# Optimization experiments

Hardware: AMD Instinct MI355X
Metric: run time of the kernel (lower is better)

The kernel has to match this reference:

```python
import jax, jax.numpy as jnp
import numpy as np

EPS = 1e-8

def setup_inputs() -> dict:
    key = jax.random.key(0)
    k1, k2 = jax.random.split(key)
    B, N, D, K = 8, 8192, 768, 256
    x = jax.random.normal(k1, (B, N, D), dtype=jnp.float32)
    centers = jax.random.normal(k2, (B, K, D), dtype=jnp.float32)
    return {"x": x, "centers": centers}

def reference(x, centers):
    # tokens_norm / centers_norm as in the torch module (add-eps normalization)
    tn = x / (jnp.linalg.norm(x, axis=-1, keepdims=True) + EPS)
    cn = centers / (jnp.linalg.norm(centers, axis=-1, keepdims=True) + EPS)
    # F.cosine_similarity re-normalizes with clamp(norm, min=eps)
    tn2 = tn / jnp.maximum(jnp.linalg.norm(tn, axis=-1, keepdims=True), EPS)
    cn2 = cn / jnp.maximum(jnp.linalg.norm(cn, axis=-1, keepdims=True), EPS)
    # fused: cosine similarity via plain matmul instead of (B,N,K,D) broadcast
    cos_sim = jnp.einsum('bnd,bkd->bnk', tn2, cn2)  # (B,N,K)
    dist = 1.0 - cos_sim
    prob = jax.nn.softmax(-dist, axis=-1)  # softmax over K
    # weighted aggregation over N: (B,K,D)
    num = jnp.einsum('bnk,bnd->bkd', prob, x)
    den = jnp.sum(prob, axis=1)[..., None] + EPS  # (B,K,1)
    return num / den
```

## Files before the change

### kernel.cpp

```cpp
#include <hip/hip_runtime.h>
#include <hip/hip_bf16.h>

typedef __attribute__((ext_vector_type(8))) short bf16x8;
typedef __attribute__((ext_vector_type(4))) float f32x4;
typedef unsigned short u16;
typedef unsigned int u32;

__device__ __forceinline__ u16 f2bf(float f) {
    u32 u = __float_as_uint(f);
    u = (u + 0x7FFFu + ((u >> 16) & 1u)) >> 16;
    return (u16)u;
}
__device__ __forceinline__ u32 pk2(float a, float b) {
    return (u32)f2bf(a) | ((u32)f2bf(b) << 16);
}

#define GLDS16(g, l) __builtin_amdgcn_global_load_lds( \
    (const __attribute__((address_space(1))) u32*)(g), \
    (__attribute__((address_space(3))) u32*)(l), 16, 0, 0)

__global__ __launch_bounds__(256) void k_centers(const float* __restrict__ c, u16* __restrict__ cn) {
    int bid = blockIdx.x;
    int w = threadIdx.x >> 6, lane = threadIdx.x & 63;
    int row = (bid << 2) + w;
    int b = row >> 8;
    __shared__ u16 rb[4][800];
    const float* src = c + (size_t)row * 768;
    float v[12]; float ss = 0.f;
#pragma unroll
    for (int j = 0; j < 12; ++j) { v[j] = src[lane + (j << 6)]; ss += v[j] * v[j]; }
#pragma unroll
    for (int m = 1; m < 64; m <<= 1) ss += __shfl_xor(ss, m, 64);
    float inv = 1.0f / sqrtf(ss);
#pragma unroll
    for (int j = 0; j < 12; ++j) rb[w][lane + (j << 6)] = f2bf(v[j] * inv);
    __syncthreads();
    int t = threadIdx.x;
    int k0 = (bid << 2) & 255;
#pragma unroll
    for (int p = 0; p < 2; ++p) {
        int idx = (p << 8) + t;
        if (idx < 384) {
            int g = idx >> 2, kr = idx & 3;
            uint4 val = *reinterpret_cast<const uint4*>(&rb[kr][g << 3]);
            int kb = g >> 2, dc = g & 3;
            size_t o = ((((size_t)(b * 24 + kb) << 2) + dc) << 8) + k0 + kr;
            *reinterpret_cast<uint4*>(cn + (o << 3)) = val;
        }
    }
}

__global__ __launch_bounds__(256, 2) void k_gemm1(const float* __restrict__ x, const u16* __restrict__ cn,
                                                  u16* __restrict__ probT, float* __restrict__ den) {
    const int b = blockIdx.y;
    const int n0 = blockIdx.x << 7;
    const int t = threadIdx.x;
    const int wave = t >> 6, lane = t & 63;
    const int lg = lane >> 4, lr = lane & 15;
    const int wm = wave >> 1, wk = wave & 1;
    const int tok0 = wm << 6;
    const int kb0 = wk << 7;

    __shared__ union {
        struct {
            u16 A[2][4][130][8];
            u16 B[2][4][256][8];
        } s;
        u16 T[256][136];
    } u;
    __shared__ float inv_s[128];
    __shared__ float ksum[2][128];
    __shared__ float denp[256];

    denp[t] = 0.f;

    f32x4 acc[8][4];
#pragma unroll
    for (int kf = 0; kf < 8; ++kf)
#pragma unroll
        for (int tf = 0; tf < 4; ++tf) acc[kf][tf] = (f32x4){0.f, 0.f, 0.f, 0.f};

    const char* cnb = (const char*)(cn + (size_t)b * 24 * 4 * 256 * 8);
    const int tokS = ((t >> 1) & 63) + ((t >> 7) << 6);
    const int dcS = t & 1;
    const float* ap = x + ((size_t)b * 8192 + n0 + tokS) * 768 + (dcS << 3);

    float sq = 0.f;
    float4 f0, f1, f2, f3;

    auto issueA = [&](int kb) {
        const float* p = ap + (kb << 5);
        f0 = *reinterpret_cast<const float4*>(p);
        f1 = *reinterpret_cast<const float4*>(p + 4);
        f2 = *reinterpret_cast<const float4*>(p + 16);
        f3 = *reinterpret_cast<const float4*>(p + 20);
    };
    auto writeA = [&](int buf) {
        sq += f0.x*f0.x + f0.y*f0.y + f0.z*f0.z + f0.w*f0.w
            + f1.x*f1.x + f1.y*f1.y + f1.z*f1.z + f1.w*f1.w
            + f2.x*f2.x + f2.y*f2.y + f2.z*f2.z + f2.w*f2.w
            + f3.x*f3.x + f3.y*f3.y + f3.z*f3.z + f3.w*f3.w;
        *reinterpret_cast<uint4*>(&u.s.A[buf][dcS][tokS][0]) =
            make_uint4(pk2(f0.x, f0.y), pk2(f0.z, f0.w), pk2(f1.x, f1.y), pk2(f1.z, f1.w));
        *reinterpret_cast<uint4*>(&u.s.A[buf][dcS + 2][tokS][0]) =
            make_uint4(pk2(f2.x, f2.y), pk2(f2.z, f2.w), pk2(f3.x, f3.y), pk2(f3.z, f3.w));
    };
    auto issueB = [&](int buf, int kb) {
        const char* src = cnb + (size_t)kb * 16384 + (wave << 12) + (lane << 4);
        char* dst = (char*)&u.s.B[buf][0][0][0] + (wave << 12);
        GLDS16(src, dst);
        GLDS16(src + 1024, dst + 1024);
        GLDS16(src + 2048, dst + 2048);
        GLDS16(src + 3072, dst + 3072);
    };

    issueA(0); issueB(0, 0);
    writeA(0);
    __syncthreads();

    for (int kb = 0; kb < 24; ++kb) {
        int cur = kb & 1, nxt = cur ^ 1;
        if (kb < 23) { issueA(kb + 1); issueB(nxt, kb + 1); }
        bf16x8 a[4];
#pragma unroll
        for (int tf = 0; tf < 4; ++tf)
            a[tf] = *reinterpret_cast<const bf16x8*>(&u.s.A[cur][lg][tok0 + (tf << 4) + lr][0]);
#pragma unroll
        for (int kf = 0; kf < 8; ++kf) {
            bf16x8 bb = *reinterpret_cast<const bf16x8*>(&u.s.B[cur][lg][kb0 + (kf << 4) + lr][0]);
#pragma unroll
            for (int tf = 0; tf < 4; ++tf)
                acc[kf][tf] = __builtin_amdgcn_mfma_f32_16x16x32_bf16(a[tf], bb, acc[kf][tf], 0, 0, 0);
        }
        if (kb < 23) writeA(nxt);
        __syncthreads();
    }

    sq += __shfl_xor(sq, 1, 64);
    if ((t & 1) == 0) inv_s[tokS] = 1.0f / sqrtf(sq);
    __syncthreads();

    float iv[4][4];
#pragma unroll
    for (int tf = 0; tf < 4; ++tf)
#pragma unroll
        for (int r = 0; r < 4; ++r)
            iv[tf][r] = inv_s[tok0 + (tf << 4) + (lg << 2) + r];

    float rowsum[4][4];
#pragma unroll
    for (int tf = 0; tf < 4; ++tf)
#pragma unroll
        for (int r = 0; r < 4; ++r) rowsum[tf][r] = 0.f;
#pragma unroll
    for (int kf = 0; kf < 8; ++kf)
#pragma unroll
        for (int tf = 0; tf < 4; ++tf)
#pragma unroll
            for (int r = 0; r < 4; ++r) {
                float e = __expf(acc[kf][tf][r] * iv[tf][r]);
                acc[kf][tf][r] = e; rowsum[tf][r] += e;
            }
#pragma unroll
    for (int tf = 0; tf < 4; ++tf)
#pragma unroll
        for (int r = 0; r < 4; ++r) {
#pragma unroll
            for (int m = 1; m < 16; m <<= 1) rowsum[tf][r] += __shfl_xor(rowsum[tf][r], m, 64);
        }
    if (lr == 0) {
#pragma unroll
        for (int tf = 0; tf < 4; ++tf)
#pragma unroll
            for (int r = 0; r < 4; ++r)
                ksum[wk][tok0 + (tf << 4) + (lg << 2) + r] = rowsum[tf][r];
    }
    __syncthreads();

    float rs[4][4];
#pragma unroll
    for (int tf = 0; tf < 4; ++tf)
#pragma unroll
        for (int r = 0; r < 4; ++r) {
            int idx = tok0 + (tf << 4) + (lg << 2) + r;
            rs[tf][r] = 1.0f / (ksum[0][idx] + ksum[1][idx]);
        }

    float dcol[8];
#pragma unroll
    for (int kf = 0; kf < 8; ++kf) dcol[kf] = 0.f;
#pragma unroll
    for (int kf = 0; kf < 8; ++kf)
#pragma unroll
        for (int tf = 0; tf < 4; ++tf)
#pragma unroll
            for (int r = 0; r < 4; ++r) {
                float p = acc[kf][tf][r] * rs[tf][r];
                acc[kf][tf][r] = p; dcol[kf] += p;
            }
#pragma unroll
    for (int kf = 0; kf < 8; ++kf) {
        dcol[kf] += __shfl_xor(dcol[kf], 16, 64);
        dcol[kf] += __shfl_xor(dcol[kf], 32, 64);
    }
    if (lg == 0) {
#pragma unroll
        for (int kf = 0; kf < 8; ++kf) atomicAdd(&denp[kb0 + (kf << 4) + lr], dcol[kf]);
    }
#pragma unroll
    for (int kf = 0; kf < 8; ++kf)
#pragma unroll
        for (int tf = 0; tf < 4; ++tf)
            *reinterpret_cast<ushort4*>(&u.T[kb0 + (kf << 4) + lr][tok0 + (tf << 4) + (lg << 2)]) =
                make_ushort4(f2bf(acc[kf][tf][0]), f2bf(acc[kf][tf][1]),
                             f2bf(acc[kf][tf][2]), f2bf(acc[kf][tf][3]));
    __syncthreads();

    u16* pTb = probT + (size_t)b * 256 * 8192 + n0;
#pragma unroll
    for (int i = 0; i < 16; ++i) {
        int idx = (i << 8) + t;
        int row = idx >> 4, ch = idx & 15;
        *reinterpret_cast<uint4*>(pTb + (size_t)row * 8192 + (ch << 3)) =
            *reinterpret_cast<const uint4*>(&u.T[row][ch << 3]);
    }
    atomicAdd(&den[(b << 8) + t], denp[t]);
}

__global__ __launch_bounds__(256) void k_gemm2(const float* __restrict__ x, const u16* __restrict__ probT,
                                               float* __restrict__ num_part) {
    const int bid = blockIdx.x;
    const int xcd = bid & 7, slot = bid >> 3;
    const int orig = xcd * 96 + slot;
    const int dt = orig % 12, sb = orig / 12;
    const int s = sb >> 3, b = sb & 7;
    const int d0 = dt << 6;
    const int t = threadIdx.x;
    const int wave = t >> 6, lane = t & 63;
    const int lg = lane >> 4, lr = lane & 15;

    f32x4 acc[4][4];
#pragma unroll
    for (int m = 0; m < 4; ++m)
#pragma unroll
        for (int tt = 0; tt < 4; ++tt) acc[m][tt] = (f32x4){0.f, 0.f, 0.f, 0.f};

    const int n0 = s << 10;
    const u16* pA = probT + (size_t)b * 256 * 8192;
    const float* xB = x + (size_t)b * 8192 * 768;

    for (int kb = 0; kb < 32; ++kb) {
        int nbase = n0 + (kb << 5);
        bf16x8 a[4];
#pragma unroll
        for (int m = 0; m < 4; ++m) {
            int k = (wave << 6) + (m << 4) + lr;
            a[m] = *reinterpret_cast<const bf16x8*>(pA + (size_t)k * 8192 + nbase + (lg << 3));
        }
        const float* xr = xB + (size_t)(nbase + (lg << 3)) * 768 + d0 + lr;
        bf16x8 bb[4];
#pragma unroll
        for (int tt = 0; tt < 4; ++tt)
#pragma unroll
            for (int j = 0; j < 8; ++j) {
                float f = xr[(size_t)j * 768 + (tt << 4)];
                bb[tt][j] = (short)f2bf(f);
            }
#pragma unroll
        for (int m = 0; m < 4; ++m)
#pragma unroll
            for (int tt = 0; tt < 4; ++tt)
                acc[m][tt] = __builtin_amdgcn_mfma_f32_16x16x32_bf16(a[m], bb[tt], acc[m][tt], 0, 0, 0);
    }

    float* np = num_part + ((size_t)s * 8 + b) * 256 * 768;
#pragma unroll
    for (int m = 0; m < 4; ++m) {
        int kb_ = (wave << 6) + (m << 4) + (lg << 2);
#pragma unroll
        for (int reg = 0; reg < 4; ++reg)
#pragma unroll
            for (int tt = 0; tt < 4; ++tt)
                np[(size_t)(kb_ + reg) * 768 + d0 + (tt << 4) + lr] = acc[m][tt][reg];
    }
}

__global__ __launch_bounds__(256) void k_final(const float* __restrict__ num_part, const float* __restrict__ den,
                                               float* __restrict__ out) {
    int i = blockIdx.x * 256 + threadIdx.x;
    float sum = 0.f;
#pragma unroll
    for (int ss = 0; ss < 8; ++ss) sum += num_part[(size_t)ss * 1572864 + i];
    out[i] = sum / (den[i / 768] + 1e-8f);
}

extern "C" void kernel_launch(void* const* d_in, const int* in_sizes, int n_in,
                              void* d_out, int out_size, void* d_ws, size_t ws_size,
                              hipStream_t stream) {
    const float* x = (const float*)d_in[0];
    const float* centers = (const float*)d_in[1];
    float* out = (float*)d_out;
    char* ws = (char*)d_ws;
    u16* cn       = (u16*)ws;
    u16* probT    = (u16*)(ws + 3145728);
    float* den    = (float*)(ws + 36700160);
    float* numpt  = (float*)(ws + 36708352);

    hipMemsetAsync(den, 0, 8192, stream);
    k_centers<<<512, 256, 0, stream>>>(centers, cn);
    k_gemm1<<<dim3(64, 8), 256, 0, stream>>>(x, cn, probT, den);
    k_gemm2<<<768, 256, 0, stream>>>(x, probT, numpt);
    k_final<<<6144, 256, 0, stream>>>(numpt, den, out);
}
```

Before: 177.8 us.

## Enlarge gemm1 token tile to 256 with triple-buffered pipeline and partial-waitcnt barriers

k_gemm1 now processes 256 tokens per block with 512 threads. Each centers tile is therefore reused across twice as many tokens, and the grid is halved. The K loop is unrolled by two over a three-slot LDS ring. Custom barriers wait only until the newest stage's global loads remain outstanding (vmcnt(6)), so loads for step k+2 overlap MFMA work on step k. The transposed output buffer grows to about 135KB of LDS, which limits occupancy to one block per CU and relies on the hand-counted vmcnt being correct.

Measured after the change: 180.7 us. Within noise of the previous version (+1.6%).

```diff
diff --git a/kernel.cpp b/kernel.cpp
--- a/kernel.cpp
+++ b/kernel.cpp
@@ -18,6 +18,11 @@
 #define GLDS16(g, l) __builtin_amdgcn_global_load_lds( \
     (const __attribute__((address_space(1))) u32*)(g), \
     (__attribute__((address_space(3))) u32*)(l), 16, 0, 0)
+
+#define BAR_CNT6() do { asm volatile("s_waitcnt vmcnt(6) lgkmcnt(0)" ::: "memory"); \
+    __builtin_amdgcn_sched_barrier(0); __builtin_amdgcn_s_barrier(); } while (0)
+#define BAR_CNT0() do { asm volatile("s_waitcnt vmcnt(0) lgkmcnt(0)" ::: "memory"); \
+    __builtin_amdgcn_sched_barrier(0); __builtin_amdgcn_s_barrier(); } while (0)
 
 __global__ __launch_bounds__(256) void k_centers(const float* __restrict__ c, u16* __restrict__ cn) {
     int bid = blockIdx.x;
@@ -50,10 +55,10 @@
     }
 }
 
-__global__ __launch_bounds__(256, 2) void k_gemm1(const float* __restrict__ x, const u16* __restrict__ cn,
+__global__ __launch_bounds__(512, 2) void k_gemm1(const float* __restrict__ x, const u16* __restrict__ cn,
                                                   u16* __restrict__ probT, float* __restrict__ den) {
     const int b = blockIdx.y;
-    const int n0 = blockIdx.x << 7;
+    const int n0 = blockIdx.x << 8;
     const int t = threadIdx.x;
     const int wave = t >> 6, lane = t & 63;
     const int lg = lane >> 4, lr = lane & 15;
@@ -63,16 +68,16 @@
 
     __shared__ union {
         struct {
-            u16 A[2][4][130][8];
-            u16 B[2][4][256][8];
+            u16 A[3][4][258][8];
+            u16 B[3][4][256][8];
         } s;
-        u16 T[256][136];
+        u16 T[256][264];
     } u;
-    __shared__ float inv_s[128];
-    __shared__ float ksum[2][128];
+    __shared__ float inv_s[256];
+    __shared__ float ksum[2][256];
     __shared__ float denp[256];
 
-    denp[t] = 0.f;
+    if (t < 256) denp[t] = 0.f;
 
     f32x4 acc[8][4];
 #pragma unroll
@@ -81,59 +86,66 @@
         for (int tf = 0; tf < 4; ++tf) acc[kf][tf] = (f32x4){0.f, 0.f, 0.f, 0.f};
 
     const char* cnb = (const char*)(cn + (size_t)b * 24 * 4 * 256 * 8);
-    const int tokS = ((t >> 1) & 63) + ((t >> 7) << 6);
+    const int tokS = t >> 1;
     const int dcS = t & 1;
-    const float* ap = x + ((size_t)b * 8192 + n0 + tokS) * 768 + (dcS << 3);
+    const float* ap = x + ((size_t)b * 8192 + n0 + tokS) * 768 + (dcS << 4);
 
     float sq = 0.f;
-    float4 f0, f1, f2, f3;
-
-    auto issueA = [&](int kb) {
+    float4 fE[4], fO[4];
+
+    auto issueA = [&](int kb, float4* f) {
         const float* p = ap + (kb << 5);
-        f0 = *reinterpret_cast<const float4*>(p);
-        f1 = *reinterpret_cast<const float4*>(p + 4);
-        f2 = *reinterpret_cast<const float4*>(p + 16);
-        f3 = *reinterpret_cast<const float4*>(p + 20);
+        f[0] = *reinterpret_cast<const float4*>(p);
+        f[1] = *reinterpret_cast<const float4*>(p + 4);
+        f[2] = *reinterpret_cast<const float4*>(p + 8);
+        f[3] = *reinterpret_cast<const float4*>(p + 12);
     };
-    auto writeA = [&](int buf) {
-        sq += f0.x*f0.x + f0.y*f0.y + f0.z*f0.z + f0.w*f0.w
-            + f1.x*f1.x + f1.y*f1.y + f1.z*f1.z + f1.w*f1.w
-            + f2.x*f2.x + f2.y*f2.y + f2.z*f2.z + f2.w*f2.w
-            + f3.x*f3.x + f3.y*f3.y + f3.z*f3.z + f3.w*f3.w;
-        *reinterpret_cast<uint4*>(&u.s.A[buf][dcS][tokS][0]) =
-            make_uint4(pk2(f0.x, f0.y), pk2(f0.z, f0.w), pk2(f1.x, f1.y), pk2(f1.z, f1.w));
-        *reinterpret_cast<uint4*>(&u.s.A[buf][dcS + 2][tokS][0]) =
-            make_uint4(pk2(f2.x, f2.y), pk2(f2.z, f2.w), pk2(f3.x, f3.y), pk2(f3.z, f3.w));
+    auto writeA = [&](int buf, float4* f) {
+#pragma unroll
+        for (int j = 0; j < 4; ++j)
+            sq += f[j].x * f[j].x + f[j].y * f[j].y + f[j].z * f[j].z + f[j].w * f[j].w;
+        *reinterpret_cast<uint4*>(&u.s.A[buf][(dcS << 1) + 0][tokS][0]) =
+            make_uint4(pk2(f[0].x, f[0].y), pk2(f[0].z, f[0].w), pk2(f[1].x, f[1].y), pk2(f[1].z, f[1].w));
+        *reinterpret_cast<uint4*>(&u.s.A[buf][(dcS << 1) + 1][tokS][0]) =
+            make_uint4(pk2(f[2].x, f[2].y), pk2(f[2].z, f[2].w), pk2(f[3].x, f[3].y), pk2(f[3].z, f[3].w));
     };
     auto issueB = [&](int buf, int kb) {
-        const char* src = cnb + (size_t)kb * 16384 + (wave << 12) + (lane << 4);
-        char* dst = (char*)&u.s.B[buf][0][0][0] + (wave << 12);
+        const char* src = cnb + (size_t)kb * 16384 + (wave << 11) + (lane << 4);
+        char* dst = (char*)&u.s.B[buf][0][0][0] + (wave << 11);
         GLDS16(src, dst);
         GLDS16(src + 1024, dst + 1024);
-        GLDS16(src + 2048, dst + 2048);
-        GLDS16(src + 3072, dst + 3072);
     };
-
-    issueA(0); issueB(0, 0);
-    writeA(0);
-    __syncthreads();
-
-    for (int kb = 0; kb < 24; ++kb) {
-        int cur = kb & 1, nxt = cur ^ 1;
-        if (kb < 23) { issueA(kb + 1); issueB(nxt, kb + 1); }
+    auto mfmaStep = [&](int buf) {
         bf16x8 a[4];
 #pragma unroll
         for (int tf = 0; tf < 4; ++tf)
-            a[tf] = *reinterpret_cast<const bf16x8*>(&u.s.A[cur][lg][tok0 + (tf << 4) + lr][0]);
+            a[tf] = *reinterpret_cast<const bf16x8*>(&u.s.A[buf][lg][tok0 + (tf << 4) + lr][0]);
 #pragma unroll
         for (int kf = 0; kf < 8; ++kf) {
-            bf16x8 bb = *reinterpret_cast<const bf16x8*>(&u.s.B[cur][lg][kb0 + (kf << 4) + lr][0]);
+            bf16x8 bb = *reinterpret_cast<const bf16x8*>(&u.s.B[buf][lg][kb0 + (kf << 4) + lr][0]);
 #pragma unroll
             for (int tf = 0; tf < 4; ++tf)
                 acc[kf][tf] = __builtin_amdgcn_mfma_f32_16x16x32_bf16(a[tf], bb, acc[kf][tf], 0, 0, 0);
         }
-        if (kb < 23) writeA(nxt);
-        __syncthreads();
+    };
+
+    issueA(0, fE); issueB(0, 0);
+    issueA(1, fO); issueB(1, 1);
+    writeA(0, fE);
+    BAR_CNT6();
+
+    for (int kb = 0; kb < 24; kb += 2) {
+        int bi0 = kb % 3, bi1 = (kb + 1) % 3, bi2 = (kb + 2) % 3;
+        if (kb < 22) { issueA(kb + 2, fE); issueB(bi2, kb + 2); }
+        mfmaStep(bi0);
+        writeA(bi1, fO);
+        BAR_CNT6();
+        if (kb < 21) { issueA(kb + 3, fO); issueB(bi0, kb + 3); }
+        mfmaStep(bi1);
+        if (kb < 22) {
+            writeA(bi2, fE);
+            if (kb == 20) { BAR_CNT0(); } else { BAR_CNT6(); }
+        }
     }
 
     sq += __shfl_xor(sq, 1, 64);
@@ -219,12 +231,12 @@
     u16* pTb = probT + (size_t)b * 256 * 8192 + n0;
 #pragma unroll
     for (int i = 0; i < 16; ++i) {
-        int idx = (i << 8) + t;
-        int row = idx >> 4, ch = idx & 15;
+        int idx = (i << 9) + t;
+        int row = idx >> 5, ch = idx & 31;
         *reinterpret_cast<uint4*>(pTb + (size_t)row * 8192 + (ch << 3)) =
             *reinterpret_cast<const uint4*>(&u.T[row][ch << 3]);
     }
-    atomicAdd(&den[(b << 8) + t], denp[t]);
+    if (t < 256) atomicAdd(&den[(b << 8) + t], denp[t]);
 }
 
 __global__ __launch_bounds__(256) void k_gemm2(const float* __restrict__ x, const u16* __restrict__ probT,
@@ -308,7 +320,7 @@
 
     hipMemsetAsync(den, 0, 8192, stream);
     k_centers<<<512, 256, 0, stream>>>(centers, cn);
-    k_gemm1<<<dim3(64, 8), 256, 0, stream>>>(x, cn, probT, den);
+    k_gemm1<<<dim3(32, 8), 512, 0, stream>>>(x, cn, probT, den);
     k_gemm2<<<768, 256, 0, stream>>>(x, probT, numpt);
     k_final<<<6144, 256, 0, stream>>>(numpt, den, out);
 }
```

## Restructure gemm1 to load operands directly into registers with smaller tiles

Applied to the files above, without the earlier changes.

Rewrites the first GEMM kernel so each block handles 64 tokens instead of 128, and each wave owns a 64-wide slice of the 256 centers. The shared-memory staging, double buffering and global_load_lds path are removed, and fragments are loaded straight from global memory into registers. The grid becomes 1024 blocks interleaved across batches, with a higher occupancy bound. This cuts LDS use and barriers to raise occupancy. In exchange, every wave re-reads the same x rows from global or cache, and loads are no longer software-pipelined.

Result: slower. 246.4 us (+38.6%).

```diff
diff --git a/kernel.cpp b/kernel.cpp
--- a/kernel.cpp
+++ b/kernel.cpp
@@ -14,10 +14,7 @@
 __device__ __forceinline__ u32 pk2(float a, float b) {
     return (u32)f2bf(a) | ((u32)f2bf(b) << 16);
 }
-
-#define GLDS16(g, l) __builtin_amdgcn_global_load_lds( \
-    (const __attribute__((address_space(1))) u32*)(g), \
-    (__attribute__((address_space(3))) u32*)(l), 16, 0, 0)
+union B8 { u32 u[4]; bf16x8 v; };
 
 __global__ __launch_bounds__(256) void k_centers(const float* __restrict__ c, u16* __restrict__ cn) {
     int bid = blockIdx.x;
@@ -50,179 +47,149 @@
     }
 }
 
-__global__ __launch_bounds__(256, 2) void k_gemm1(const float* __restrict__ x, const u16* __restrict__ cn,
+__global__ __launch_bounds__(256, 3) void k_gemm1(const float* __restrict__ x, const u16* __restrict__ cn,
                                                   u16* __restrict__ probT, float* __restrict__ den) {
-    const int b = blockIdx.y;
-    const int n0 = blockIdx.x << 7;
+    const int bid = blockIdx.x;
+    const int b = bid & 7;
+    const int n0 = (bid >> 3) << 6;
     const int t = threadIdx.x;
     const int wave = t >> 6, lane = t & 63;
     const int lg = lane >> 4, lr = lane & 15;
-    const int wm = wave >> 1, wk = wave & 1;
-    const int tok0 = wm << 6;
-    const int kb0 = wk << 7;
-
-    __shared__ union {
-        struct {
-            u16 A[2][4][130][8];
-            u16 B[2][4][256][8];
-        } s;
-        u16 T[256][136];
-    } u;
-    __shared__ float inv_s[128];
-    __shared__ float ksum[2][128];
+    const int kq = wave << 6;
+
+    __shared__ u16 T[256][72];
+    __shared__ float inv_s[64];
+    __shared__ float ksum[4][64];
     __shared__ float denp[256];
 
-    denp[t] = 0.f;
-
-    f32x4 acc[8][4];
-#pragma unroll
-    for (int kf = 0; kf < 8; ++kf)
-#pragma unroll
-        for (int tf = 0; tf < 4; ++tf) acc[kf][tf] = (f32x4){0.f, 0.f, 0.f, 0.f};
-
-    const char* cnb = (const char*)(cn + (size_t)b * 24 * 4 * 256 * 8);
-    const int tokS = ((t >> 1) & 63) + ((t >> 7) << 6);
-    const int dcS = t & 1;
-    const float* ap = x + ((size_t)b * 8192 + n0 + tokS) * 768 + (dcS << 3);
-
-    float sq = 0.f;
-    float4 f0, f1, f2, f3;
-
-    auto issueA = [&](int kb) {
-        const float* p = ap + (kb << 5);
-        f0 = *reinterpret_cast<const float4*>(p);
-        f1 = *reinterpret_cast<const float4*>(p + 4);
-        f2 = *reinterpret_cast<const float4*>(p + 16);
-        f3 = *reinterpret_cast<const float4*>(p + 20);
-    };
-    auto writeA = [&](int buf) {
-        sq += f0.x*f0.x + f0.y*f0.y + f0.z*f0.z + f0.w*f0.w
-            + f1.x*f1.x + f1.y*f1.y + f1.z*f1.z + f1.w*f1.w
-            + f2.x*f2.x + f2.y*f2.y + f2.z*f2.z + f2.w*f2.w
-            + f3.x*f3.x + f3.y*f3.y + f3.z*f3.z + f3.w*f3.w;
-        *reinterpret_cast<uint4*>(&u.s.A[buf][dcS][tokS][0]) =
-            make_uint4(pk2(f0.x, f0.y), pk2(f0.z, f0.w), pk2(f1.x, f1.y), pk2(f1.z, f1.w));
-        *reinterpret_cast<uint4*>(&u.s.A[buf][dcS + 2][tokS][0]) =
-            make_uint4(pk2(f2.x, f2.y), pk2(f2.z, f2.w), pk2(f3.x, f3.y), pk2(f3.z, f3.w));
-    };
-    auto issueB = [&](int buf, int kb) {
-        const char* src = cnb + (size_t)kb * 16384 + (wave << 12) + (lane << 4);
-        char* dst = (char*)&u.s.B[buf][0][0][0] + (wave << 12);
-        GLDS16(src, dst);
-        GLDS16(src + 1024, dst + 1024);
-        GLDS16(src + 2048, dst + 2048);
-        GLDS16(src + 3072, dst + 3072);
-    };
-
-    issueA(0); issueB(0, 0);
-    writeA(0);
-    __syncthreads();
-
-    for (int kb = 0; kb < 24; ++kb) {
-        int cur = kb & 1, nxt = cur ^ 1;
-        if (kb < 23) { issueA(kb + 1); issueB(nxt, kb + 1); }
-        bf16x8 a[4];
+    f32x4 acc[4][4];
+#pragma unroll
+    for (int tf = 0; tf < 4; ++tf)
+#pragma unroll
+        for (int kf = 0; kf < 4; ++kf) acc[tf][kf] = (f32x4){0.f, 0.f, 0.f, 0.f};
+
+    const float* xb = x + ((size_t)b * 8192 + n0) * 768;
+    const u16* cnb = cn + (size_t)b * 24 * 4 * 256 * 8;
+
+    float sq[4] = {0.f, 0.f, 0.f, 0.f};
+
+#pragma unroll 2
+    for (int st = 0; st < 24; ++st) {
+        bf16x8 bf[4];
+#pragma unroll
+        for (int kf = 0; kf < 4; ++kf)
+            bf[kf] = *reinterpret_cast<const bf16x8*>(
+                cnb + (((size_t)(st << 2) + lg) * 256 + kq + (kf << 4) + lr) * 8);
+        bf16x8 af[4];
+#pragma unroll
+        for (int tf = 0; tf < 4; ++tf) {
+            const float* p = xb + (size_t)((tf << 4) + lr) * 768 + (st << 5) + (lg << 3);
+            float4 f0 = *reinterpret_cast<const float4*>(p);
+            float4 f1 = *reinterpret_cast<const float4*>(p + 4);
+            sq[tf] += f0.x*f0.x + f0.y*f0.y + f0.z*f0.z + f0.w*f0.w
+                    + f1.x*f1.x + f1.y*f1.y + f1.z*f1.z + f1.w*f1.w;
+            B8 a;
+            a.u[0] = pk2(f0.x, f0.y); a.u[1] = pk2(f0.z, f0.w);
+            a.u[2] = pk2(f1.x, f1.y); a.u[3] = pk2(f1.z, f1.w);
+            af[tf] = a.v;
+        }
 #pragma unroll
         for (int tf = 0; tf < 4; ++tf)
-            a[tf] = *reinterpret_cast<const bf16x8*>(&u.s.A[cur][lg][tok0 + (tf << 4) + lr][0]);
-#pragma unroll
-        for (int kf = 0; kf < 8; ++kf) {
-            bf16x8 bb = *reinterpret_cast<const bf16x8*>(&u.s.B[cur][lg][kb0 + (kf << 4) + lr][0]);
-#pragma unroll
-            for (int tf = 0; tf < 4; ++tf)
-                acc[kf][tf] = __builtin_amdgcn_mfma_f32_16x16x32_bf16(a[tf], bb, acc[kf][tf], 0, 0, 0);
-        }
-        if (kb < 23) writeA(nxt);
-        __syncthreads();
-    }
-
-    sq += __shfl_xor(sq, 1, 64);
-    if ((t & 1) == 0) inv_s[tokS] = 1.0f / sqrtf(sq);
+#pragma unroll
+            for (int kf = 0; kf < 4; ++kf)
+                acc[tf][kf] = __builtin_amdgcn_mfma_f32_16x16x32_bf16(af[tf], bf[kf], acc[tf][kf], 0, 0, 0);
+    }
+
+#pragma unroll
+    for (int tf = 0; tf < 4; ++tf) {
+        sq[tf] += __shfl_xor(sq[tf], 16, 64);
+        sq[tf] += __shfl_xor(sq[tf], 32, 64);
+    }
+    if (wave == 0 && lane < 16) {
+#pragma unroll
+        for (int tf = 0; tf < 4; ++tf) inv_s[(tf << 4) + lr] = 1.0f / sqrtf(sq[tf]);
+    }
     __syncthreads();
 
     float iv[4][4];
 #pragma unroll
     for (int tf = 0; tf < 4; ++tf)
 #pragma unroll
-        for (int r = 0; r < 4; ++r)
-            iv[tf][r] = inv_s[tok0 + (tf << 4) + (lg << 2) + r];
-
-    float rowsum[4][4];
-#pragma unroll
-    for (int tf = 0; tf < 4; ++tf)
-#pragma unroll
-        for (int r = 0; r < 4; ++r) rowsum[tf][r] = 0.f;
-#pragma unroll
-    for (int kf = 0; kf < 8; ++kf)
+        for (int r = 0; r < 4; ++r) iv[tf][r] = inv_s[(tf << 4) + (lg << 2) + r];
+
+    float rsum[4][4];
+#pragma unroll
+    for (int tf = 0; tf < 4; ++tf)
+#pragma unroll
+        for (int r = 0; r < 4; ++r) rsum[tf][r] = 0.f;
+#pragma unroll
+    for (int tf = 0; tf < 4; ++tf)
+#pragma unroll
+        for (int kf = 0; kf < 4; ++kf)
+#pragma unroll
+            for (int r = 0; r < 4; ++r) {
+                float e = __expf(acc[tf][kf][r] * iv[tf][r]);
+                acc[tf][kf][r] = e; rsum[tf][r] += e;
+            }
+#pragma unroll
+    for (int tf = 0; tf < 4; ++tf)
+#pragma unroll
+        for (int r = 0; r < 4; ++r) {
+#pragma unroll
+            for (int m = 1; m < 16; m <<= 1) rsum[tf][r] += __shfl_xor(rsum[tf][r], m, 64);
+        }
+    if (lr == 0) {
 #pragma unroll
         for (int tf = 0; tf < 4; ++tf)
 #pragma unroll
+            for (int r = 0; r < 4; ++r) ksum[wave][(tf << 4) + (lg << 2) + r] = rsum[tf][r];
+    }
+    __syncthreads();
+
+    float rs[4][4];
+#pragma unroll
+    for (int tf = 0; tf < 4; ++tf)
+#pragma unroll
+        for (int r = 0; r < 4; ++r) {
+            int i = (tf << 4) + (lg << 2) + r;
+            rs[tf][r] = 1.0f / (ksum[0][i] + ksum[1][i] + ksum[2][i] + ksum[3][i]);
+        }
+
+    float dcol[4] = {0.f, 0.f, 0.f, 0.f};
+#pragma unroll
+    for (int tf = 0; tf < 4; ++tf)
+#pragma unroll
+        for (int kf = 0; kf < 4; ++kf)
+#pragma unroll
             for (int r = 0; r < 4; ++r) {
-                float e = __expf(acc[kf][tf][r] * iv[tf][r]);
-                acc[kf][tf][r] = e; rowsum[tf][r] += e;
+                float p = acc[tf][kf][r] * rs[tf][r];
+                acc[tf][kf][r] = p; dcol[kf] += p;
             }
 #pragma unroll
-    for (int tf = 0; tf < 4; ++tf)
-#pragma unroll
-        for (int r = 0; r < 4; ++r) {
-#pragma unroll
-            for (int m = 1; m < 16; m <<= 1) rowsum[tf][r] += __shfl_xor(rowsum[tf][r], m, 64);
-        }
-    if (lr == 0) {
-#pragma unroll
-        for (int tf = 0; tf < 4; ++tf)
-#pragma unroll
-            for (int r = 0; r < 4; ++r)
-                ksum[wk][tok0 + (tf << 4) + (lg << 2) + r] = rowsum[tf][r];
-    }
-    __syncthreads();
-
-    float rs[4][4];
-#pragma unroll
-    for (int tf = 0; tf < 4; ++tf)
-#pragma unroll
-        for (int r = 0; r < 4; ++r) {
-            int idx = tok0 + (tf << 4) + (lg << 2) + r;
-            rs[tf][r] = 1.0f / (ksum[0][idx] + ksum[1][idx]);
-        }
-
-    float dcol[8];
-#pragma unroll
-    for (int kf = 0; kf < 8; ++kf) dcol[kf] = 0.f;
-#pragma unroll
-    for (int kf = 0; kf < 8; ++kf)
-#pragma unroll
-        for (int tf = 0; tf < 4; ++tf)
-#pragma unroll
-            for (int r = 0; r < 4; ++r) {
-                float p = acc[kf][tf][r] * rs[tf][r];
-                acc[kf][tf][r] = p; dcol[kf] += p;
-            }
-#pragma unroll
-    for (int kf = 0; kf < 8; ++kf) {
+    for (int kf = 0; kf < 4; ++kf) {
         dcol[kf] += __shfl_xor(dcol[kf], 16, 64);
         dcol[kf] += __shfl_xor(dcol[kf], 32, 64);
     }
     if (lg == 0) {
 #pragma unroll
-        for (int kf = 0; kf < 8; ++kf) atomicAdd(&denp[kb0 + (kf << 4) + lr], dcol[kf]);
-    }
-#pragma unroll
-    for (int kf = 0; kf < 8; ++kf)
-#pragma unroll
-        for (int tf = 0; tf < 4; ++tf)
-            *reinterpret_cast<ushort4*>(&u.T[kb0 + (kf << 4) + lr][tok0 + (tf << 4) + (lg << 2)]) =
-                make_ushort4(f2bf(acc[kf][tf][0]), f2bf(acc[kf][tf][1]),
-                             f2bf(acc[kf][tf][2]), f2bf(acc[kf][tf][3]));
+        for (int kf = 0; kf < 4; ++kf) denp[kq + (kf << 4) + lr] = dcol[kf];
+    }
+#pragma unroll
+    for (int tf = 0; tf < 4; ++tf)
+#pragma unroll
+        for (int kf = 0; kf < 4; ++kf)
+            *reinterpret_cast<ushort4*>(&T[kq + (kf << 4) + lr][(tf << 4) + (lg << 2)]) =
+                make_ushort4(f2bf(acc[tf][kf][0]), f2bf(acc[tf][kf][1]),
+                             f2bf(acc[tf][kf][2]), f2bf(acc[tf][kf][3]));
     __syncthreads();
 
     u16* pTb = probT + (size_t)b * 256 * 8192 + n0;
 #pragma unroll
-    for (int i = 0; i < 16; ++i) {
+    for (int i = 0; i < 8; ++i) {
         int idx = (i << 8) + t;
-        int row = idx >> 4, ch = idx & 15;
+        int row = idx >> 3, ch = idx & 7;
         *reinterpret_cast<uint4*>(pTb + (size_t)row * 8192 + (ch << 3)) =
-            *reinterpret_cast<const uint4*>(&u.T[row][ch << 3]);
+            *reinterpret_cast<const uint4*>(&T[row][ch << 3]);
     }
     atomicAdd(&den[(b << 8) + t], denp[t]);
 }
@@ -308,7 +275,7 @@
 
     hipMemsetAsync(den, 0, 8192, stream);
     k_centers<<<512, 256, 0, stream>>>(centers, cn);
-    k_gemm1<<<dim3(64, 8), 256, 0, stream>>>(x, cn, probT, den);
+    k_gemm1<<<1024, 256, 0, stream>>>(x, cn, probT, den);
     k_gemm2<<<768, 256, 0, stream>>>(x, probT, numpt);
     k_final<<<6144, 256, 0, stream>>>(numpt, den, out);
 }
```

## Replace split-N PV GEMM and reduction kernel with single fused PV kernel

Applied to the files above, without the earlier changes.

Rewrites the second GEMM so each block covers a 64-center by 32-column tile over all tokens, accumulating in registers and dividing by the softmax denominator in the epilogue. This removes the partial-sum buffer writes and the separate reduction kernel launch. In exchange each block runs a long serial loop with only two MFMAs per step, and x and probT are re-read more times across blocks with less reuse per load.

New measurement: 307.6 us. 1.73x slower.

```diff
diff --git a/kernel.cpp b/kernel.cpp
--- a/kernel.cpp
+++ b/kernel.cpp
@@ -227,71 +227,52 @@
     atomicAdd(&den[(b << 8) + t], denp[t]);
 }
 
-__global__ __launch_bounds__(256) void k_gemm2(const float* __restrict__ x, const u16* __restrict__ probT,
-                                               float* __restrict__ num_part) {
+__global__ __launch_bounds__(256) void k_pv(const float* __restrict__ x, const u16* __restrict__ probT,
+                                            const float* __restrict__ den, float* __restrict__ out) {
     const int bid = blockIdx.x;
-    const int xcd = bid & 7, slot = bid >> 3;
-    const int orig = xcd * 96 + slot;
-    const int dt = orig % 12, sb = orig / 12;
-    const int s = sb >> 3, b = sb & 7;
-    const int d0 = dt << 6;
+    const int b = bid & 7;
+    const int slot = bid >> 3;
+    const int kq = slot & 3;
+    const int d0 = (slot >> 2) << 5;
     const int t = threadIdx.x;
     const int wave = t >> 6, lane = t & 63;
     const int lg = lane >> 4, lr = lane & 15;
-
-    f32x4 acc[4][4];
-#pragma unroll
-    for (int m = 0; m < 4; ++m)
-#pragma unroll
-        for (int tt = 0; tt < 4; ++tt) acc[m][tt] = (f32x4){0.f, 0.f, 0.f, 0.f};
-
-    const int n0 = s << 10;
-    const u16* pA = probT + (size_t)b * 256 * 8192;
-    const float* xB = x + (size_t)b * 8192 * 768;
-
-    for (int kb = 0; kb < 32; ++kb) {
-        int nbase = n0 + (kb << 5);
-        bf16x8 a[4];
-#pragma unroll
-        for (int m = 0; m < 4; ++m) {
-            int k = (wave << 6) + (m << 4) + lr;
-            a[m] = *reinterpret_cast<const bf16x8*>(pA + (size_t)k * 8192 + nbase + (lg << 3));
-        }
-        const float* xr = xB + (size_t)(nbase + (lg << 3)) * 768 + d0 + lr;
-        bf16x8 bb[4];
-#pragma unroll
-        for (int tt = 0; tt < 4; ++tt)
-#pragma unroll
-            for (int j = 0; j < 8; ++j) {
-                float f = xr[(size_t)j * 768 + (tt << 4)];
-                bb[tt][j] = (short)f2bf(f);
-            }
-#pragma unroll
-        for (int m = 0; m < 4; ++m)
-#pragma unroll
-            for (int tt = 0; tt < 4; ++tt)
-                acc[m][tt] = __builtin_amdgcn_mfma_f32_16x16x32_bf16(a[m], bb[tt], acc[m][tt], 0, 0, 0);
-    }
-
-    float* np = num_part + ((size_t)s * 8 + b) * 256 * 768;
-#pragma unroll
-    for (int m = 0; m < 4; ++m) {
-        int kb_ = (wave << 6) + (m << 4) + (lg << 2);
-#pragma unroll
-        for (int reg = 0; reg < 4; ++reg)
-#pragma unroll
-            for (int tt = 0; tt < 4; ++tt)
-                np[(size_t)(kb_ + reg) * 768 + d0 + (tt << 4) + lr] = acc[m][tt][reg];
-    }
-}
-
-__global__ __launch_bounds__(256) void k_final(const float* __restrict__ num_part, const float* __restrict__ den,
-                                               float* __restrict__ out) {
-    int i = blockIdx.x * 256 + threadIdx.x;
-    float sum = 0.f;
-#pragma unroll
-    for (int ss = 0; ss < 8; ++ss) sum += num_part[(size_t)ss * 1572864 + i];
-    out[i] = sum / (den[i / 768] + 1e-8f);
+    const int k0 = (kq << 6) + (wave << 4);
+
+    f32x4 acc[2];
+    acc[0] = (f32x4){0.f, 0.f, 0.f, 0.f};
+    acc[1] = (f32x4){0.f, 0.f, 0.f, 0.f};
+
+    const u16* pA = probT + (size_t)b * 256 * 8192 + (size_t)(k0 + lr) * 8192 + (lg << 3);
+    const float* xB = x + (size_t)b * 8192 * 768 + (size_t)(lg << 3) * 768 + d0 + lr;
+
+#pragma unroll 2
+    for (int nb = 0; nb < 256; ++nb) {
+        const int n = nb << 5;
+        bf16x8 a = *reinterpret_cast<const bf16x8*>(pA + n);
+        const float* xr = xB + (size_t)n * 768;
+        bf16x8 b0, b1;
+#pragma unroll
+        for (int j = 0; j < 8; ++j) {
+            float v0 = xr[(size_t)j * 768];
+            float v1 = xr[(size_t)j * 768 + 16];
+            b0[j] = (short)f2bf(v0);
+            b1[j] = (short)f2bf(v1);
+        }
+        acc[0] = __builtin_amdgcn_mfma_f32_16x16x32_bf16(a, b0, acc[0], 0, 0, 0);
+        acc[1] = __builtin_amdgcn_mfma_f32_16x16x32_bf16(a, b1, acc[1], 0, 0, 0);
+    }
+
+    float dv[4];
+#pragma unroll
+    for (int r = 0; r < 4; ++r)
+        dv[r] = 1.0f / (den[(b << 8) + k0 + (lg << 2) + r] + 1e-8f);
+    float* ob = out + ((size_t)(b << 8) + k0 + (lg << 2)) * 768 + d0 + lr;
+#pragma unroll
+    for (int r = 0; r < 4; ++r) {
+        ob[(size_t)r * 768] = acc[0][r] * dv[r];
+        ob[(size_t)r * 768 + 16] = acc[1][r] * dv[r];
+    }
 }
 
 extern "C" void kernel_launch(void* const* d_in, const int* in_sizes, int n_in,
@@ -304,11 +285,9 @@
     u16* cn       = (u16*)ws;
     u16* probT    = (u16*)(ws + 3145728);
     float* den    = (float*)(ws + 36700160);
-    float* numpt  = (float*)(ws + 36708352);
 
     hipMemsetAsync(den, 0, 8192, stream);
     k_centers<<<512, 256, 0, stream>>>(centers, cn);
     k_gemm1<<<dim3(64, 8), 256, 0, stream>>>(x, cn, probT, den);
-    k_gemm2<<<768, 256, 0, stream>>>(x, probT, numpt);
-    k_final<<<6144, 256, 0, stream>>>(numpt, den, out);
-}
+    k_pv<<<768, 256, 0, stream>>>(x, probT, den, out);
+}
```
